# Performance work log

Hardware: AMD Instinct MI355X
Metric: run time of the kernel (lower is better)

The kernel has to match this reference:

```python
import jax, jax.numpy as jnp
import numpy as np


def _gcn_conv(x, src, dst, W, b, num_nodes, deg_inv_sqrt):
    # PyG GCNConv: h = x @ W, then normalized scatter-add over edges (incl. self loops), + bias
    h = x @ W  # [N, d_out]
    norm = deg_inv_sqrt[src] * deg_inv_sqrt[dst]  # [E']
    msg = h[src] * norm[:, None]  # gather + scale, [E', d_out]
    out = jax.ops.segment_sum(msg, dst, num_segments=num_nodes)  # scatter-add to targets
    return out + b


def reference(x, edge_index, W1, b1, W2, b2, num_nodes):
    src0, dst0 = edge_index[0], edge_index[1]
    loop = jnp.arange(num_nodes, dtype=edge_index.dtype)
    # add self loops (PyG default add_self_loops=True)
    src = jnp.concatenate([src0, loop])
    dst = jnp.concatenate([dst0, loop])
    # symmetric normalization D^{-1/2} (A+I) D^{-1/2}, degree from self-looped graph
    deg = jax.ops.segment_sum(jnp.ones_like(src, dtype=x.dtype), dst, num_segments=num_nodes)
    deg_inv_sqrt = jnp.where(deg > 0, jax.lax.rsqrt(jnp.maximum(deg, 1)), 0.0).astype(x.dtype)

    z = jax.nn.relu(_gcn_conv(x, src, dst, W1, b1, num_nodes, deg_inv_sqrt))
    z = jax.nn.relu(_gcn_conv(z, src, dst, W2, b2, num_nodes, deg_inv_sqrt))
    return z


def setup_inputs() -> dict:
    key = jax.random.key(0)
    k1, k2, k3, k4 = jax.random.split(key, 4)
    N, E, D, H = 50000, 1600000, 128, 128
    x = jax.random.normal(k1, (N, D), dtype=jnp.float32)
    edge_index = jax.random.randint(k2, (2, E), 0, N, dtype=jnp.int64)
    s = 1.0 / np.sqrt(D)
    W1 = jax.random.normal(k3, (D, H), dtype=jnp.float32) * s
    W2 = jax.random.normal(k4, (H, H), dtype=jnp.float32) * s
    return {
        "x": x,
        "edge_index": edge_index,
        "W1": W1,
        "b1": jnp.zeros((H,), jnp.float32),
        "W2": W2,
        "b2": jnp.zeros((H,), jnp.float32),
        "num_nodes": N,
    }
```

## Files before the change

### kernel.cpp

```cpp
#include <hip/hip_runtime.h>

#define FD 128
#define BSH 7
#define CH 4096
#define CHT 16
#define KMAX 512
#define SCAP 8192

typedef __attribute__((ext_vector_type(8))) short bf16x8;
typedef __attribute__((ext_vector_type(4))) float f32x4;

__device__ inline unsigned bfr(float f) {
    unsigned u = __float_as_uint(f);
    return (u + 0x7FFF + ((u >> 16) & 1)) >> 16;
}
__device__ inline float uplo(unsigned p) { return __uint_as_float(p << 16); }
__device__ inline float uphi(unsigned p) { return __uint_as_float(p & 0xFFFF0000u); }


__global__ __launch_bounds__(256) void partition_kernel(
        const int* __restrict__ src, const int* __restrict__ dst,
        int* __restrict__ lstartG, int* __restrict__ total,
        int* __restrict__ pairs, int E, int K) {
    __shared__ int lcnt[KMAX];
    __shared__ int lstart[KMAX];
    __shared__ int sm[256];
    __shared__ int staged[CH];
    int t = threadIdx.x;
    int base = blockIdx.x * CH;
    int n = min(CH, E - base);

    lcnt[t] = 0; lcnt[t + 256] = 0;
    __syncthreads();

    int pk[CHT]; int bn[CHT];
    #pragma unroll
    for (int j = 0; j < CHT; ++j) {
        int i = t + j * 256;
        bn[j] = -1;
        if (i < n) {
            int d = dst[base + i];
            int s = src[base + i];
            bn[j] = d >> BSH;
            pk[j] = ((d & ((1 << BSH) - 1)) << 17) | s;
            atomicAdd(&lcnt[bn[j]], 1);
        }
    }
    __syncthreads();

    int c0 = lcnt[2 * t], c1 = lcnt[2 * t + 1];
    int s2 = c0 + c1;
    sm[t] = s2;
    __syncthreads();
    for (int off = 1; off < 256; off <<= 1) {
        int add = (t >= off) ? sm[t - off] : 0;
        __syncthreads();
        sm[t] += add;
        __syncthreads();
    }
    int ex = sm[t] - s2;
    lstart[2 * t] = ex;     lstart[2 * t + 1] = ex + c0;
    lcnt[2 * t]   = ex;     lcnt[2 * t + 1]   = ex + c0;
    __syncthreads();

    #pragma unroll
    for (int j = 0; j < CHT; ++j) {
        if (bn[j] >= 0) {
            int pos = atomicAdd(&lcnt[bn[j]], 1);
            staged[pos] = pk[j];
        }
    }
    __syncthreads();

    for (int i = t; i < n; i += 256)
        pairs[base + i] = staged[i];

    size_t lrow = (size_t)blockIdx.x * (K + 1);
    for (int b = t; b < K; b += 256) {
        lstartG[lrow + b] = lstart[b];
        int c = lcnt[b] - lstart[b];
        if (c) atomicAdd(&total[b], c);
    }
    if (t == 0) lstartG[lrow + K] = n;
}

__global__ __launch_bounds__(512) void trtot_kernel(
        const int* __restrict__ A, int* __restrict__ B, int R, int C,
        const int* __restrict__ total, int* __restrict__ bbase,
        int* __restrict__ rp, int K, int E, int N, int nbx) {
    __shared__ int tile[32][33];
    int t = threadIdx.x;
    if ((int)blockIdx.x == gridDim.x - 1) {
        __shared__ int sm[512];
        int v = (t < K) ? total[t] : 0;
        sm[t] = v;
        __syncthreads();
        for (int off = 1; off < 512; off <<= 1) {
            int add = (t >= off) ? sm[t - off] : 0;
            __syncthreads();
            sm[t] += add;
            __syncthreads();
        }
        if (t < K) bbase[t] = sm[t] - v;
        if (t == 0) { bbase[K] = E; rp[N] = E; }
        return;
    }
    int c0 = (blockIdx.x % nbx) * 32, r0 = (blockIdx.x / nbx) * 32;
    int tx = t & 31, ty = t >> 5;
    for (int i = ty; i < 32; i += 16) {
        int r = r0 + i, c = c0 + tx;
        if (r < R && c < C) tile[i][tx] = A[(size_t)r * C + c];
    }
    __syncthreads();
    for (int i = ty; i < 32; i += 16) {
        int c = c0 + i, r = r0 + tx;
        if (c < C && r < R) B[(size_t)c * R + r] = tile[tx][i];
    }
}

__global__ __launch_bounds__(256) void build_kernel(
        const int* __restrict__ pairs, const int* __restrict__ lstartT,
        const int* __restrict__ bbase, int* __restrict__ rp,
        float* __restrict__ dis, int* __restrict__ col, int N, int PB, int K,
        const float* __restrict__ W1, unsigned short* __restrict__ W1T,
        const float* __restrict__ W2, unsigned short* __restrict__ W2T) {
    __shared__ int staged[SCAP];
    __shared__ int lcnt[512];
    __shared__ int pref[512];
    __shared__ int sm[256];
    int b = blockIdx.x;
    int t = threadIdx.x;

    if (b >= K) {
        int bb = b - K;
        #pragma unroll
        for (int rr = 0; rr < 2; ++rr) {
            int f = bb * 512 + rr * 256 + t;
            int w = f >> 14, rm = f & 16383, k = rm >> 7, nn2 = rm & 127;
            const float* W = w ? W2 : W1;
            unsigned short* WT = w ? W2T : W1T;
            WT[nn2 * FD + k] = (unsigned short)bfr(W[k * FD + nn2]);
        }
        return;
    }

    int wv = t >> 6;
    int nbase = b << BSH;
    int nn = min(1 << BSH, N - nbase);
    int beg = bbase[b];
    int cnt = bbase[b + 1] - beg;

    int fp[2], fl0[2], flen[2];
    int nf = 0, mysum = 0;
    for (int p = t; p < PB; p += 256) {
        int l0 = lstartT[(size_t)b * PB + p];
        int l1 = lstartT[(size_t)(b + 1) * PB + p];
        fp[nf] = p; fl0[nf] = l0; flen[nf] = l1 - l0;
        mysum += l1 - l0;
        ++nf;
    }
    sm[t] = mysum;
    __syncthreads();
    for (int off = 1; off < 256; off <<= 1) {
        int add = (t >= off) ? sm[t - off] : 0;
        __syncthreads();
        sm[t] += add;
        __syncthreads();
    }
    int o = sm[t] - mysum;

    lcnt[t] = 0; lcnt[t + 256] = 0;
    __syncthreads();

    if (cnt <= SCAP) {
        int oo = o;
        for (int f = 0; f < nf; ++f) {
            int gbase = fp[f] * CH + fl0[f];
            for (int i = 0; i < flen[f]; ++i) {
                int p = pairs[gbase + i];
                staged[oo + i] = p;
                atomicAdd(&lcnt[((p >> 17) << 2) | wv], 1);
            }
            oo += flen[f];
        }
    } else {
        for (int f = 0; f < nf; ++f) {
            int gbase = fp[f] * CH + fl0[f];
            for (int i = 0; i < flen[f]; ++i)
                atomicAdd(&lcnt[((pairs[gbase + i] >> 17) << 2) | wv], 1);
        }
    }
    __syncthreads();

    int c0 = lcnt[2 * t], c1 = lcnt[2 * t + 1];
    int s2 = c0 + c1;
    sm[t] = s2;
    __syncthreads();
    for (int off = 1; off < 256; off <<= 1) {
        int add = (t >= off) ? sm[t - off] : 0;
        __syncthreads();
        sm[t] += add;
        __syncthreads();
    }
    int ex = sm[t] - s2;
    pref[2 * t] = ex;  pref[2 * t + 1] = ex + c0;
    __syncthreads();

    if (t < 128 && t < nn) {
        int rs = pref[t << 2];
        int re = (t < 127) ? pref[(t + 1) << 2] : cnt;
        rp[nbase + t] = beg + rs;
        dis[nbase + t] = rsqrtf((float)(re - rs + 1));
    }
    lcnt[2 * t]     = beg + pref[2 * t];
    lcnt[2 * t + 1] = beg + pref[2 * t + 1];
    __syncthreads();

    if (cnt <= SCAP) {
        int oo = o;
        for (int f = 0; f < nf; ++f) {
            for (int i = 0; i < flen[f]; ++i) {
                int p = staged[oo + i];
                int pos = atomicAdd(&lcnt[((p >> 17) << 2) | wv], 1);
                col[pos] = p & 0x1FFFF;
            }
            oo += flen[f];
        }
    } else {
        for (int f = 0; f < nf; ++f) {
            int gbase = fp[f] * CH + fl0[f];
            for (int i = 0; i < flen[f]; ++i) {
                int p = pairs[gbase + i];
                int pos = atomicAdd(&lcnt[((p >> 17) << 2) | wv], 1);
                col[pos] = p & 0x1FFFF;
            }
        }
    }
}


#define APAD 8
#define ASTR (FD + APAD)

template <bool A32>
__device__ void gemm_body(const void* __restrict__ Ap,
                          const unsigned short* __restrict__ WT,
                          const float* __restrict__ dis,
                          unsigned short* __restrict__ C, int M) {
    __shared__ unsigned short Bs[128 * ASTR];
    int tid = threadIdx.x;
    int lane = tid & 63;
    int wave = tid >> 6;
    int quad = lane >> 4;
    int l16 = lane & 15;
    int rowBase = blockIdx.x * 128;

    #pragma unroll
    for (int p = 0; p < 8; ++p) {
        int r = p * 16 + (tid >> 4);
        int cq = (tid & 15) * 8;
        *(uint4*)&Bs[r * ASTR + cq] = *(const uint4*)&WT[(size_t)r * FD + cq];
    }
    __syncthreads();

    int m0 = wave * 32;
    int r0 = rowBase + m0 + l16;
    int r1 = r0 + 16;
    f32x4 acc[2][8] = {};
    #pragma unroll
    for (int kt = 0; kt < 4; ++kt) {
        int ko = kt * 32 + quad * 8;
        uint4 va = make_uint4(0u, 0u, 0u, 0u);
        uint4 vb = make_uint4(0u, 0u, 0u, 0u);
        if (A32) {
            const float* A = (const float*)Ap;
            if (r0 < M) {
                const float* a = A + (size_t)r0 * FD + ko;
                float4 f0 = *(const float4*)a;
                float4 f1 = *(const float4*)(a + 4);
                va.x = bfr(f0.x) | (bfr(f0.y) << 16);
                va.y = bfr(f0.z) | (bfr(f0.w) << 16);
                va.z = bfr(f1.x) | (bfr(f1.y) << 16);
                va.w = bfr(f1.z) | (bfr(f1.w) << 16);
            }
            if (r1 < M) {
                const float* a = A + (size_t)r1 * FD + ko;
                float4 f0 = *(const float4*)a;
                float4 f1 = *(const float4*)(a + 4);
                vb.x = bfr(f0.x) | (bfr(f0.y) << 16);
                vb.y = bfr(f0.z) | (bfr(f0.w) << 16);
                vb.z = bfr(f1.x) | (bfr(f1.y) << 16);
                vb.w = bfr(f1.z) | (bfr(f1.w) << 16);
            }
        } else {
            const unsigned short* A = (const unsigned short*)Ap;
            if (r0 < M) va = *(const uint4*)(A + (size_t)r0 * FD + ko);
            if (r1 < M) vb = *(const uint4*)(A + (size_t)r1 * FD + ko);
        }
        bf16x8 a0 = *(bf16x8*)&va;
        bf16x8 a1 = *(bf16x8*)&vb;
        #pragma unroll
        for (int n = 0; n < 8; ++n) {
            bf16x8 b = *(bf16x8*)&Bs[(n * 16 + l16) * ASTR + ko];
            acc[0][n] = __builtin_amdgcn_mfma_f32_16x16x32_bf16(a0, b, acc[0][n], 0, 0, 0);
            acc[1][n] = __builtin_amdgcn_mfma_f32_16x16x32_bf16(a1, b, acc[1][n], 0, 0, 0);
        }
    }

    #pragma unroll
    for (int ms = 0; ms < 2; ++ms) {
        #pragma unroll
        for (int r = 0; r < 4; ++r) {
            int grow = rowBase + m0 + ms * 16 + quad * 4 + r;
            if (grow < M) {
                float dv = dis[grow];
                #pragma unroll
                for (int n = 0; n < 8; ++n) {
                    C[(size_t)grow * FD + n * 16 + l16] =
                        (unsigned short)bfr(dv * acc[ms][n][r]);
                }
            }
        }
    }
}

__global__ __launch_bounds__(256) void gemm_mfma_f32(
        const float* __restrict__ A, const unsigned short* __restrict__ WT,
        const float* __restrict__ dis, unsigned short* __restrict__ C, int M) {
    gemm_body<true>(A, WT, dis, C, M);
}

__global__ __launch_bounds__(256) void gemm_mfma_bf16(
        const unsigned short* __restrict__ A, const unsigned short* __restrict__ WT,
        const float* __restrict__ dis, unsigned short* __restrict__ C, int M) {
    gemm_body<false>(A, WT, dis, C, M);
}


__global__ __launch_bounds__(256) void agg_kernel(
        const unsigned* __restrict__ h, const float* __restrict__ dis,
        const int* __restrict__ rp, const int* __restrict__ col,
        const float2* __restrict__ bias, void* __restrict__ out, int N, int obf) {
    int v = blockIdx.x * 4 + threadIdx.y;
    v = __builtin_amdgcn_readfirstlane(v);
    if (v >= N) return;
    int t = threadIdx.x;
    float dv = dis[v];
    size_t vb = (size_t)v * 64 + t;
    unsigned hp = h[vb];
    float2 acc;
    acc.x = uplo(hp); acc.y = uphi(hp);
    int e = rp[v];
    int end = rp[v + 1];

    for (; e + 16 <= end; e += 16) {
        int u[16];
        #pragma unroll
        for (int j = 0; j < 16; ++j) u[j] = col[e + j];
        unsigned p[16];
        #pragma unroll
        for (int j = 0; j < 16; ++j) p[j] = h[(size_t)u[j] * 64 + t];
        #pragma unroll
        for (int j = 0; j < 16; ++j) {
            acc.x += uplo(p[j]); acc.y += uphi(p[j]);
        }
    }
    for (; e + 4 <= end; e += 4) {
        int u0 = col[e], u1 = col[e + 1], u2 = col[e + 2], u3 = col[e + 3];
        unsigned p0 = h[(size_t)u0 * 64 + t];
        unsigned p1 = h[(size_t)u1 * 64 + t];
        unsigned p2 = h[(size_t)u2 * 64 + t];
        unsigned p3 = h[(size_t)u3 * 64 + t];
        acc.x += uplo(p0); acc.y += uphi(p0);
        acc.x += uplo(p1); acc.y += uphi(p1);
        acc.x += uplo(p2); acc.y += uphi(p2);
        acc.x += uplo(p3); acc.y += uphi(p3);
    }
    for (; e < end; ++e) {
        unsigned p = h[(size_t)col[e] * 64 + t];
        acc.x += uplo(p); acc.y += uphi(p);
    }

    float2 bb = bias[t];
    float2 r;
    r.x = fmaxf(fmaf(dv, acc.x, bb.x), 0.0f);
    r.y = fmaxf(fmaf(dv, acc.y, bb.y), 0.0f);
    if (obf) {
        ((unsigned*)out)[vb] = bfr(r.x) | (bfr(r.y) << 16);
    } else {
        ((float2*)out)[vb] = r;
    }
}


extern "C" void kernel_launch(void* const* d_in, const int* in_sizes, int n_in,
                              void* d_out, int out_size, void* d_ws, size_t ws_size,
                              hipStream_t stream) {
    const float* x  = (const float*)d_in[0];
    const int*   ei = (const int*)d_in[1];
    const float* W1 = (const float*)d_in[2];
    const float* b1 = (const float*)d_in[3];
    const float* W2 = (const float*)d_in[4];
    const float* b2 = (const float*)d_in[5];

    int N = in_sizes[0] / FD;
    int E = in_sizes[1] / 2;
    const int* src = ei;
    const int* dst = ei + E;
    int K = (N + (1 << BSH) - 1) >> BSH;
    int PB = (E + CH - 1) / CH;

    char* base = (char*)d_ws;
    size_t off = 0;
    auto align256 = [](size_t v) { return (v + 255) & ~(size_t)255; };
    int*            rp    = (int*)(base + off);            off += align256((size_t)(N + 1) * 4);
    float*          dis   = (float*)(base + off);          off += align256((size_t)N * 4);
    int*            total = (int*)(base + off);            off += align256(512 * 4);
    int*            bbase = (int*)(base + off);            off += align256(513 * 4);
    unsigned short* w1t   = (unsigned short*)(base + off); off += align256((size_t)FD * FD * 2);
    unsigned short* w2t   = (unsigned short*)(base + off); off += align256((size_t)FD * FD * 2);
    int*            col   = (int*)(base + off);            off += align256((size_t)E * 4);
    unsigned short* hbuf  = (unsigned short*)(base + off); off += align256((size_t)N * FD * 2);
    unsigned short* z1    = (unsigned short*)(base + off); off += align256((size_t)N * FD * 2);
    int*            pairs = (int*)(base + off);            off += align256((size_t)E * 4);
    int*            lstartG = (int*)hbuf;
    int*            lstartT = (int*)z1;
    (void)ws_size; (void)n_in; (void)out_size;

    (void)hipMemsetAsync(total, 0, 512 * 4, stream);
    partition_kernel<<<PB, 256, 0, stream>>>(src, dst, lstartG, total, pairs, E, K);
    int nbx = (K + 1 + 31) / 32;
    int nby = (PB + 31) / 32;
    trtot_kernel<<<nbx * nby + 1, 512, 0, stream>>>(lstartG, lstartT, PB, K + 1,
                                                    total, bbase, rp, K, E, N, nbx);
    build_kernel<<<K + 64, 256, 0, stream>>>(pairs, lstartT, bbase, rp, dis, col,
                                             N, PB, K, W1, w1t, W2, w2t);

    dim3 aggBlk(64, 4);
    int aggGrid = (N + 3) / 4;
    int gemmGrid = (N + 127) / 128;

    gemm_mfma_f32 <<<gemmGrid, 256, 0, stream>>>(x, w1t, dis, hbuf, N);
    agg_kernel<<<aggGrid, aggBlk, 0, stream>>>((const unsigned*)hbuf, dis, rp, col,
                                               (const float2*)b1, z1, N, 1);
    gemm_mfma_bf16<<<gemmGrid, 256, 0, stream>>>(z1, w2t, dis, hbuf, N);
    agg_kernel<<<aggGrid, aggBlk, 0, stream>>>((const unsigned*)hbuf, dis, rp, col,
                                               (const float2*)b2, d_out, N, 0);
}
```

Baseline: 245.4 us.

## Compute degrees with atomics and fuse layer-1 GEMM into CSR build kernel

Node degrees are now counted with global atomics in extra blocks of the partition kernel, and the inverse square roots plus the weight transposes move into extra blocks of the transpose kernel. Because the normalisation no longer depends on the CSR build, the first-layer GEMM runs as extra blocks of the build kernel, so it overlaps the column scatter and one launch is removed. In exchange it adds 1.6M random global atomics and a larger memset. The GEMM blocks also inherit the build kernel's bigger shared-memory allocation, which may lower their occupancy.

```diff
diff --git a/kernel.cpp b/kernel.cpp
--- a/kernel.cpp
+++ b/kernel.cpp
@@ -6,6 +6,7 @@
 #define CHT 16
 #define KMAX 512
 #define SCAP 8192
+#define DB 128
 
 typedef __attribute__((ext_vector_type(8))) short bf16x8;
 typedef __attribute__((ext_vector_type(4))) float f32x4;
@@ -21,12 +22,21 @@
 __global__ __launch_bounds__(256) void partition_kernel(
         const int* __restrict__ src, const int* __restrict__ dst,
         int* __restrict__ lstartG, int* __restrict__ total,
-        int* __restrict__ pairs, int E, int K) {
+        int* __restrict__ pairs, int E, int K, int PB,
+        int* __restrict__ deg) {
     __shared__ int lcnt[KMAX];
     __shared__ int lstart[KMAX];
     __shared__ int sm[256];
     __shared__ int staged[CH];
     int t = threadIdx.x;
+
+    if ((int)blockIdx.x >= PB) {
+        int i0 = ((int)blockIdx.x - PB) * 256 + t;
+        for (int i = i0; i < E; i += DB * 256)
+            atomicAdd(&deg[dst[i]], 1);
+        return;
+    }
+
     int base = blockIdx.x * CH;
     int n = min(CH, E - base);
 
@@ -87,10 +97,14 @@
 __global__ __launch_bounds__(512) void trtot_kernel(
         const int* __restrict__ A, int* __restrict__ B, int R, int C,
         const int* __restrict__ total, int* __restrict__ bbase,
-        int* __restrict__ rp, int K, int E, int N, int nbx) {
+        int* __restrict__ rp, int K, int E, int N, int nbx, int nbt, int ndis,
+        const int* __restrict__ deg, float* __restrict__ dis,
+        const float* __restrict__ W1, unsigned short* __restrict__ W1T,
+        const float* __restrict__ W2, unsigned short* __restrict__ W2T) {
     __shared__ int tile[32][33];
     int t = threadIdx.x;
-    if ((int)blockIdx.x == gridDim.x - 1) {
+    int b = blockIdx.x;
+    if (b == nbt) {
         __shared__ int sm[512];
         int v = (t < K) ? total[t] : 0;
         sm[t] = v;
@@ -105,7 +119,21 @@
         if (t == 0) { bbase[K] = E; rp[N] = E; }
         return;
     }
-    int c0 = (blockIdx.x % nbx) * 32, r0 = (blockIdx.x / nbx) * 32;
+    if (b > nbt) {
+        int i = b - nbt - 1;
+        if (i < ndis) {
+            int v = i * 512 + t;
+            if (v < N) dis[v] = rsqrtf((float)(deg[v] + 1));
+        } else {
+            int f = (i - ndis) * 512 + t;
+            int w = f >> 14, rm = f & 16383, k = rm >> 7, nn2 = rm & 127;
+            const float* W = w ? W2 : W1;
+            unsigned short* WT = w ? W2T : W1T;
+            WT[nn2 * FD + k] = (unsigned short)bfr(W[k * FD + nn2]);
+        }
+        return;
+    }
+    int c0 = (b % nbx) * 32, r0 = (b / nbx) * 32;
     int tx = t & 31, ty = t >> 5;
     for (int i = ty; i < 32; i += 16) {
         int r = r0 + i, c = c0 + tx;
@@ -118,142 +146,22 @@
     }
 }
 
-__global__ __launch_bounds__(256) void build_kernel(
-        const int* __restrict__ pairs, const int* __restrict__ lstartT,
-        const int* __restrict__ bbase, int* __restrict__ rp,
-        float* __restrict__ dis, int* __restrict__ col, int N, int PB, int K,
-        const float* __restrict__ W1, unsigned short* __restrict__ W1T,
-        const float* __restrict__ W2, unsigned short* __restrict__ W2T) {
-    __shared__ int staged[SCAP];
-    __shared__ int lcnt[512];
-    __shared__ int pref[512];
-    __shared__ int sm[256];
-    int b = blockIdx.x;
-    int t = threadIdx.x;
-
-    if (b >= K) {
-        int bb = b - K;
-        #pragma unroll
-        for (int rr = 0; rr < 2; ++rr) {
-            int f = bb * 512 + rr * 256 + t;
-            int w = f >> 14, rm = f & 16383, k = rm >> 7, nn2 = rm & 127;
-            const float* W = w ? W2 : W1;
-            unsigned short* WT = w ? W2T : W1T;
-            WT[nn2 * FD + k] = (unsigned short)bfr(W[k * FD + nn2]);
-        }
-        return;
-    }
-
-    int wv = t >> 6;
-    int nbase = b << BSH;
-    int nn = min(1 << BSH, N - nbase);
-    int beg = bbase[b];
-    int cnt = bbase[b + 1] - beg;
-
-    int fp[2], fl0[2], flen[2];
-    int nf = 0, mysum = 0;
-    for (int p = t; p < PB; p += 256) {
-        int l0 = lstartT[(size_t)b * PB + p];
-        int l1 = lstartT[(size_t)(b + 1) * PB + p];
-        fp[nf] = p; fl0[nf] = l0; flen[nf] = l1 - l0;
-        mysum += l1 - l0;
-        ++nf;
-    }
-    sm[t] = mysum;
-    __syncthreads();
-    for (int off = 1; off < 256; off <<= 1) {
-        int add = (t >= off) ? sm[t - off] : 0;
-        __syncthreads();
-        sm[t] += add;
-        __syncthreads();
-    }
-    int o = sm[t] - mysum;
-
-    lcnt[t] = 0; lcnt[t + 256] = 0;
-    __syncthreads();
-
-    if (cnt <= SCAP) {
-        int oo = o;
-        for (int f = 0; f < nf; ++f) {
-            int gbase = fp[f] * CH + fl0[f];
-            for (int i = 0; i < flen[f]; ++i) {
-                int p = pairs[gbase + i];
-                staged[oo + i] = p;
-                atomicAdd(&lcnt[((p >> 17) << 2) | wv], 1);
-            }
-            oo += flen[f];
-        }
-    } else {
-        for (int f = 0; f < nf; ++f) {
-            int gbase = fp[f] * CH + fl0[f];
-            for (int i = 0; i < flen[f]; ++i)
-                atomicAdd(&lcnt[((pairs[gbase + i] >> 17) << 2) | wv], 1);
-        }
-    }
-    __syncthreads();
-
-    int c0 = lcnt[2 * t], c1 = lcnt[2 * t + 1];
-    int s2 = c0 + c1;
-    sm[t] = s2;
-    __syncthreads();
-    for (int off = 1; off < 256; off <<= 1) {
-        int add = (t >= off) ? sm[t - off] : 0;
-        __syncthreads();
-        sm[t] += add;
-        __syncthreads();
-    }
-    int ex = sm[t] - s2;
-    pref[2 * t] = ex;  pref[2 * t + 1] = ex + c0;
-    __syncthreads();
-
-    if (t < 128 && t < nn) {
-        int rs = pref[t << 2];
-        int re = (t < 127) ? pref[(t + 1) << 2] : cnt;
-        rp[nbase + t] = beg + rs;
-        dis[nbase + t] = rsqrtf((float)(re - rs + 1));
-    }
-    lcnt[2 * t]     = beg + pref[2 * t];
-    lcnt[2 * t + 1] = beg + pref[2 * t + 1];
-    __syncthreads();
-
-    if (cnt <= SCAP) {
-        int oo = o;
-        for (int f = 0; f < nf; ++f) {
-            for (int i = 0; i < flen[f]; ++i) {
-                int p = staged[oo + i];
-                int pos = atomicAdd(&lcnt[((p >> 17) << 2) | wv], 1);
-                col[pos] = p & 0x1FFFF;
-            }
-            oo += flen[f];
-        }
-    } else {
-        for (int f = 0; f < nf; ++f) {
-            int gbase = fp[f] * CH + fl0[f];
-            for (int i = 0; i < flen[f]; ++i) {
-                int p = pairs[gbase + i];
-                int pos = atomicAdd(&lcnt[((p >> 17) << 2) | wv], 1);
-                col[pos] = p & 0x1FFFF;
-            }
-        }
-    }
-}
-
 
 #define APAD 8
 #define ASTR (FD + APAD)
 
 template <bool A32>
-__device__ void gemm_body(const void* __restrict__ Ap,
+__device__ void gemm_body(unsigned short* __restrict__ Bs,
+                          const void* __restrict__ Ap,
                           const unsigned short* __restrict__ WT,
                           const float* __restrict__ dis,
-                          unsigned short* __restrict__ C, int M) {
-    __shared__ unsigned short Bs[128 * ASTR];
+                          unsigned short* __restrict__ C, int M, int blk) {
     int tid = threadIdx.x;
     int lane = tid & 63;
     int wave = tid >> 6;
     int quad = lane >> 4;
     int l16 = lane & 15;
-    int rowBase = blockIdx.x * 128;
+    int rowBase = blk * 128;
 
     #pragma unroll
     for (int p = 0; p < 8; ++p) {
@@ -324,16 +232,123 @@
     }
 }
 
-__global__ __launch_bounds__(256) void gemm_mfma_f32(
-        const float* __restrict__ A, const unsigned short* __restrict__ WT,
-        const float* __restrict__ dis, unsigned short* __restrict__ C, int M) {
-    gemm_body<true>(A, WT, dis, C, M);
+__global__ __launch_bounds__(256) void build_kernel(
+        const int* __restrict__ pairs, const int* __restrict__ lstartT,
+        const int* __restrict__ bbase, int* __restrict__ rp,
+        int* __restrict__ col, int N, int PB, int K,
+        const float* __restrict__ x, const unsigned short* __restrict__ w1t,
+        const float* __restrict__ dis, unsigned short* __restrict__ hbuf) {
+    __shared__ __align__(16) int smem[SCAP + 512 + 512 + 256];
+    int b = blockIdx.x;
+    int t = threadIdx.x;
+
+    if (b >= K) {
+        gemm_body<true>((unsigned short*)smem, x, w1t, dis, hbuf, N, b - K);
+        return;
+    }
+
+    int* staged = smem;
+    int* lcnt   = smem + SCAP;
+    int* pref   = smem + SCAP + 512;
+    int* sm     = smem + SCAP + 1024;
+
+    int wv = t >> 6;
+    int nbase = b << BSH;
+    int nn = min(1 << BSH, N - nbase);
+    int beg = bbase[b];
+    int cnt = bbase[b + 1] - beg;
+
+    int fp[2], fl0[2], flen[2];
+    int nf = 0, mysum = 0;
+    for (int p = t; p < PB; p += 256) {
+        int l0 = lstartT[(size_t)b * PB + p];
+        int l1 = lstartT[(size_t)(b + 1) * PB + p];
+        fp[nf] = p; fl0[nf] = l0; flen[nf] = l1 - l0;
+        mysum += l1 - l0;
+        ++nf;
+    }
+    sm[t] = mysum;
+    __syncthreads();
+    for (int off = 1; off < 256; off <<= 1) {
+        int add = (t >= off) ? sm[t - off] : 0;
+        __syncthreads();
+        sm[t] += add;
+        __syncthreads();
+    }
+    int o = sm[t] - mysum;
+
+    lcnt[t] = 0; lcnt[t + 256] = 0;
+    __syncthreads();
+
+    if (cnt <= SCAP) {
+        int oo = o;
+        for (int f = 0; f < nf; ++f) {
+            int gbase = fp[f] * CH + fl0[f];
+            for (int i = 0; i < flen[f]; ++i) {
+                int p = pairs[gbase + i];
+                staged[oo + i] = p;
+                atomicAdd(&lcnt[((p >> 17) << 2) | wv], 1);
+            }
+            oo += flen[f];
+        }
+    } else {
+        for (int f = 0; f < nf; ++f) {
+            int gbase = fp[f] * CH + fl0[f];
+            for (int i = 0; i < flen[f]; ++i)
+                atomicAdd(&lcnt[((pairs[gbase + i] >> 17) << 2) | wv], 1);
+        }
+    }
+    __syncthreads();
+
+    int c0 = lcnt[2 * t], c1 = lcnt[2 * t + 1];
+    int s2 = c0 + c1;
+    sm[t] = s2;
+    __syncthreads();
+    for (int off = 1; off < 256; off <<= 1) {
+        int add = (t >= off) ? sm[t - off] : 0;
+        __syncthreads();
+        sm[t] += add;
+        __syncthreads();
+    }
+    int ex = sm[t] - s2;
+    pref[2 * t] = ex;  pref[2 * t + 1] = ex + c0;
+    __syncthreads();
+
+    if (t < 128 && t < nn) {
+        int rs = pref[t << 2];
+        rp[nbase + t] = beg + rs;
+    }
+    lcnt[2 * t]     = beg + pref[2 * t];
+    lcnt[2 * t + 1] = beg + pref[2 * t + 1];
+    __syncthreads();
+
+    if (cnt <= SCAP) {
+        int oo = o;
+        for (int f = 0; f < nf; ++f) {
+            for (int i = 0; i < flen[f]; ++i) {
+                int p = staged[oo + i];
+                int pos = atomicAdd(&lcnt[((p >> 17) << 2) | wv], 1);
+                col[pos] = p & 0x1FFFF;
+            }
+            oo += flen[f];
+        }
+    } else {
+        for (int f = 0; f < nf; ++f) {
+            int gbase = fp[f] * CH + fl0[f];
+            for (int i = 0; i < flen[f]; ++i) {
+                int p = pairs[gbase + i];
+                int pos = atomicAdd(&lcnt[((p >> 17) << 2) | wv], 1);
+                col[pos] = p & 0x1FFFF;
+            }
+        }
+    }
 }
 
 __global__ __launch_bounds__(256) void gemm_mfma_bf16(
         const unsigned short* __restrict__ A, const unsigned short* __restrict__ WT,
         const float* __restrict__ dis, unsigned short* __restrict__ C, int M) {
-    gemm_body<false>(A, WT, dis, C, M);
+    __shared__ __align__(16) unsigned short Bs[128 * ASTR];
+    gemm_body<false>(Bs, A, WT, dis, C, M, blockIdx.x);
 }
 
 
@@ -416,6 +431,7 @@
     int*            rp    = (int*)(base + off);            off += align256((size_t)(N + 1) * 4);
     float*          dis   = (float*)(base + off);          off += align256((size_t)N * 4);
     int*            total = (int*)(base + off);            off += align256(512 * 4);
+    int*            deg   = (int*)(base + off);            off += align256((size_t)N * 4);
     int*            bbase = (int*)(base + off);            off += align256(513 * 4);
     unsigned short* w1t   = (unsigned short*)(base + off); off += align256((size_t)FD * FD * 2);
     unsigned short* w2t   = (unsigned short*)(base + off); off += align256((size_t)FD * FD * 2);
@@ -427,20 +443,25 @@
     int*            lstartT = (int*)z1;
     (void)ws_size; (void)n_in; (void)out_size;
 
-    (void)hipMemsetAsync(total, 0, 512 * 4, stream);
-    partition_kernel<<<PB, 256, 0, stream>>>(src, dst, lstartG, total, pairs, E, K);
+    (void)hipMemsetAsync(total, 0, 2048 + (size_t)N * 4, stream);
+    partition_kernel<<<PB + DB, 256, 0, stream>>>(src, dst, lstartG, total,
+                                                  pairs, E, K, PB, deg);
     int nbx = (K + 1 + 31) / 32;
     int nby = (PB + 31) / 32;
-    trtot_kernel<<<nbx * nby + 1, 512, 0, stream>>>(lstartG, lstartT, PB, K + 1,
-                                                    total, bbase, rp, K, E, N, nbx);
-    build_kernel<<<K + 64, 256, 0, stream>>>(pairs, lstartT, bbase, rp, dis, col,
-                                             N, PB, K, W1, w1t, W2, w2t);
+    int nbt = nbx * nby;
+    int ndis = (N + 511) / 512;
+    trtot_kernel<<<nbt + 1 + ndis + 64, 512, 0, stream>>>(
+        lstartG, lstartT, PB, K + 1, total, bbase, rp, K, E, N, nbx, nbt, ndis,
+        deg, dis, W1, w1t, W2, w2t);
+
+    int gemmGrid = (N + 127) / 128;
+    build_kernel<<<K + gemmGrid, 256, 0, stream>>>(pairs, lstartT, bbase, rp,
+                                                   col, N, PB, K,
+                                                   x, w1t, dis, hbuf);
 
     dim3 aggBlk(64, 4);
     int aggGrid = (N + 3) / 4;
-    int gemmGrid = (N + 127) / 128;
-
-    gemm_mfma_f32 <<<gemmGrid, 256, 0, stream>>>(x, w1t, dis, hbuf, N);
+
     agg_kernel<<<aggGrid, aggBlk, 0, stream>>>((const unsigned*)hbuf, dis, rp, col,
                                                (const float2*)b1, z1, N, 1);
     gemm_mfma_bf16<<<gemmGrid, 256, 0, stream>>>(z1, w2t, dis, hbuf, N);
```

After: 300.0 us. 1.22x slower.

## Fuse layer-1 GEMM into partition kernel and move degree scaling into aggregation

Applied to the files above, without the earlier changes.

The first-layer GEMM no longer needs the degree normalization, because the source-side scale is applied per edge inside the first aggregation (gathering dis[u] alongside h). That lets the x@W1 GEMM run as extra blocks in the same launch as edge partitioning, overlapping compute with the graph build. The weight transpose moves to a small separate kernel, and lstartG gets its own workspace region instead of aliasing hbuf. In exchange, the first aggregation does an extra random dis load and an FMA per edge, and the bf16 rounding of h now happens before scaling.

```diff
diff --git a/kernel.cpp b/kernel.cpp
--- a/kernel.cpp
+++ b/kernel.cpp
@@ -18,242 +18,21 @@
 __device__ inline float uphi(unsigned p) { return __uint_as_float(p & 0xFFFF0000u); }
 
 
-__global__ __launch_bounds__(256) void partition_kernel(
-        const int* __restrict__ src, const int* __restrict__ dst,
-        int* __restrict__ lstartG, int* __restrict__ total,
-        int* __restrict__ pairs, int E, int K) {
-    __shared__ int lcnt[KMAX];
-    __shared__ int lstart[KMAX];
-    __shared__ int sm[256];
-    __shared__ int staged[CH];
-    int t = threadIdx.x;
-    int base = blockIdx.x * CH;
-    int n = min(CH, E - base);
-
-    lcnt[t] = 0; lcnt[t + 256] = 0;
-    __syncthreads();
-
-    int pk[CHT]; int bn[CHT];
-    #pragma unroll
-    for (int j = 0; j < CHT; ++j) {
-        int i = t + j * 256;
-        bn[j] = -1;
-        if (i < n) {
-            int d = dst[base + i];
-            int s = src[base + i];
-            bn[j] = d >> BSH;
-            pk[j] = ((d & ((1 << BSH) - 1)) << 17) | s;
-            atomicAdd(&lcnt[bn[j]], 1);
-        }
-    }
-    __syncthreads();
-
-    int c0 = lcnt[2 * t], c1 = lcnt[2 * t + 1];
-    int s2 = c0 + c1;
-    sm[t] = s2;
-    __syncthreads();
-    for (int off = 1; off < 256; off <<= 1) {
-        int add = (t >= off) ? sm[t - off] : 0;
-        __syncthreads();
-        sm[t] += add;
-        __syncthreads();
-    }
-    int ex = sm[t] - s2;
-    lstart[2 * t] = ex;     lstart[2 * t + 1] = ex + c0;
-    lcnt[2 * t]   = ex;     lcnt[2 * t + 1]   = ex + c0;
-    __syncthreads();
-
-    #pragma unroll
-    for (int j = 0; j < CHT; ++j) {
-        if (bn[j] >= 0) {
-            int pos = atomicAdd(&lcnt[bn[j]], 1);
-            staged[pos] = pk[j];
-        }
-    }
-    __syncthreads();
-
-    for (int i = t; i < n; i += 256)
-        pairs[base + i] = staged[i];
-
-    size_t lrow = (size_t)blockIdx.x * (K + 1);
-    for (int b = t; b < K; b += 256) {
-        lstartG[lrow + b] = lstart[b];
-        int c = lcnt[b] - lstart[b];
-        if (c) atomicAdd(&total[b], c);
-    }
-    if (t == 0) lstartG[lrow + K] = n;
-}
-
-__global__ __launch_bounds__(512) void trtot_kernel(
-        const int* __restrict__ A, int* __restrict__ B, int R, int C,
-        const int* __restrict__ total, int* __restrict__ bbase,
-        int* __restrict__ rp, int K, int E, int N, int nbx) {
-    __shared__ int tile[32][33];
-    int t = threadIdx.x;
-    if ((int)blockIdx.x == gridDim.x - 1) {
-        __shared__ int sm[512];
-        int v = (t < K) ? total[t] : 0;
-        sm[t] = v;
-        __syncthreads();
-        for (int off = 1; off < 512; off <<= 1) {
-            int add = (t >= off) ? sm[t - off] : 0;
-            __syncthreads();
-            sm[t] += add;
-            __syncthreads();
-        }
-        if (t < K) bbase[t] = sm[t] - v;
-        if (t == 0) { bbase[K] = E; rp[N] = E; }
-        return;
-    }
-    int c0 = (blockIdx.x % nbx) * 32, r0 = (blockIdx.x / nbx) * 32;
-    int tx = t & 31, ty = t >> 5;
-    for (int i = ty; i < 32; i += 16) {
-        int r = r0 + i, c = c0 + tx;
-        if (r < R && c < C) tile[i][tx] = A[(size_t)r * C + c];
-    }
-    __syncthreads();
-    for (int i = ty; i < 32; i += 16) {
-        int c = c0 + i, r = r0 + tx;
-        if (c < C && r < R) B[(size_t)c * R + r] = tile[tx][i];
-    }
-}
-
-__global__ __launch_bounds__(256) void build_kernel(
-        const int* __restrict__ pairs, const int* __restrict__ lstartT,
-        const int* __restrict__ bbase, int* __restrict__ rp,
-        float* __restrict__ dis, int* __restrict__ col, int N, int PB, int K,
-        const float* __restrict__ W1, unsigned short* __restrict__ W1T,
-        const float* __restrict__ W2, unsigned short* __restrict__ W2T) {
-    __shared__ int staged[SCAP];
-    __shared__ int lcnt[512];
-    __shared__ int pref[512];
-    __shared__ int sm[256];
-    int b = blockIdx.x;
-    int t = threadIdx.x;
-
-    if (b >= K) {
-        int bb = b - K;
-        #pragma unroll
-        for (int rr = 0; rr < 2; ++rr) {
-            int f = bb * 512 + rr * 256 + t;
-            int w = f >> 14, rm = f & 16383, k = rm >> 7, nn2 = rm & 127;
-            const float* W = w ? W2 : W1;
-            unsigned short* WT = w ? W2T : W1T;
-            WT[nn2 * FD + k] = (unsigned short)bfr(W[k * FD + nn2]);
-        }
-        return;
-    }
-
-    int wv = t >> 6;
-    int nbase = b << BSH;
-    int nn = min(1 << BSH, N - nbase);
-    int beg = bbase[b];
-    int cnt = bbase[b + 1] - beg;
-
-    int fp[2], fl0[2], flen[2];
-    int nf = 0, mysum = 0;
-    for (int p = t; p < PB; p += 256) {
-        int l0 = lstartT[(size_t)b * PB + p];
-        int l1 = lstartT[(size_t)(b + 1) * PB + p];
-        fp[nf] = p; fl0[nf] = l0; flen[nf] = l1 - l0;
-        mysum += l1 - l0;
-        ++nf;
-    }
-    sm[t] = mysum;
-    __syncthreads();
-    for (int off = 1; off < 256; off <<= 1) {
-        int add = (t >= off) ? sm[t - off] : 0;
-        __syncthreads();
-        sm[t] += add;
-        __syncthreads();
-    }
-    int o = sm[t] - mysum;
-
-    lcnt[t] = 0; lcnt[t + 256] = 0;
-    __syncthreads();
-
-    if (cnt <= SCAP) {
-        int oo = o;
-        for (int f = 0; f < nf; ++f) {
-            int gbase = fp[f] * CH + fl0[f];
-            for (int i = 0; i < flen[f]; ++i) {
-                int p = pairs[gbase + i];
-                staged[oo + i] = p;
-                atomicAdd(&lcnt[((p >> 17) << 2) | wv], 1);
-            }
-            oo += flen[f];
-        }
-    } else {
-        for (int f = 0; f < nf; ++f) {
-            int gbase = fp[f] * CH + fl0[f];
-            for (int i = 0; i < flen[f]; ++i)
-                atomicAdd(&lcnt[((pairs[gbase + i] >> 17) << 2) | wv], 1);
-        }
-    }
-    __syncthreads();
-
-    int c0 = lcnt[2 * t], c1 = lcnt[2 * t + 1];
-    int s2 = c0 + c1;
-    sm[t] = s2;
-    __syncthreads();
-    for (int off = 1; off < 256; off <<= 1) {
-        int add = (t >= off) ? sm[t - off] : 0;
-        __syncthreads();
-        sm[t] += add;
-        __syncthreads();
-    }
-    int ex = sm[t] - s2;
-    pref[2 * t] = ex;  pref[2 * t + 1] = ex + c0;
-    __syncthreads();
-
-    if (t < 128 && t < nn) {
-        int rs = pref[t << 2];
-        int re = (t < 127) ? pref[(t + 1) << 2] : cnt;
-        rp[nbase + t] = beg + rs;
-        dis[nbase + t] = rsqrtf((float)(re - rs + 1));
-    }
-    lcnt[2 * t]     = beg + pref[2 * t];
-    lcnt[2 * t + 1] = beg + pref[2 * t + 1];
-    __syncthreads();
-
-    if (cnt <= SCAP) {
-        int oo = o;
-        for (int f = 0; f < nf; ++f) {
-            for (int i = 0; i < flen[f]; ++i) {
-                int p = staged[oo + i];
-                int pos = atomicAdd(&lcnt[((p >> 17) << 2) | wv], 1);
-                col[pos] = p & 0x1FFFF;
-            }
-            oo += flen[f];
-        }
-    } else {
-        for (int f = 0; f < nf; ++f) {
-            int gbase = fp[f] * CH + fl0[f];
-            for (int i = 0; i < flen[f]; ++i) {
-                int p = pairs[gbase + i];
-                int pos = atomicAdd(&lcnt[((p >> 17) << 2) | wv], 1);
-                col[pos] = p & 0x1FFFF;
-            }
-        }
-    }
-}
-
-
 #define APAD 8
 #define ASTR (FD + APAD)
 
-template <bool A32>
-__device__ void gemm_body(const void* __restrict__ Ap,
+template <bool A32, bool SCALE>
+__device__ void gemm_body(unsigned short* __restrict__ Bs,
+                          const void* __restrict__ Ap,
                           const unsigned short* __restrict__ WT,
                           const float* __restrict__ dis,
-                          unsigned short* __restrict__ C, int M) {
-    __shared__ unsigned short Bs[128 * ASTR];
+                          unsigned short* __restrict__ C, int M, int blk) {
     int tid = threadIdx.x;
     int lane = tid & 63;
     int wave = tid >> 6;
     int quad = lane >> 4;
     int l16 = lane & 15;
-    int rowBase = blockIdx.x * 128;
+    int rowBase = blk * 128;
 
     #pragma unroll
     for (int p = 0; p < 8; ++p) {
@@ -313,34 +92,253 @@
         for (int r = 0; r < 4; ++r) {
             int grow = rowBase + m0 + ms * 16 + quad * 4 + r;
             if (grow < M) {
-                float dv = dis[grow];
+                float dv = SCALE ? dis[grow] : 1.0f;
                 #pragma unroll
                 for (int n = 0; n < 8; ++n) {
-                    C[(size_t)grow * FD + n * 16 + l16] =
-                        (unsigned short)bfr(dv * acc[ms][n][r]);
+                    float val = SCALE ? (dv * acc[ms][n][r]) : acc[ms][n][r];
+                    C[(size_t)grow * FD + n * 16 + l16] = (unsigned short)bfr(val);
                 }
             }
         }
     }
 }
 
-__global__ __launch_bounds__(256) void gemm_mfma_f32(
-        const float* __restrict__ A, const unsigned short* __restrict__ WT,
-        const float* __restrict__ dis, unsigned short* __restrict__ C, int M) {
-    gemm_body<true>(A, WT, dis, C, M);
+__global__ void wt_kernel(const float* __restrict__ W1, unsigned short* __restrict__ W1T,
+                          const float* __restrict__ W2, unsigned short* __restrict__ W2T) {
+    int k = blockIdx.x & (FD - 1);
+    int n = threadIdx.x;
+    if (blockIdx.x < FD) W1T[n * FD + k] = (unsigned short)bfr(W1[k * FD + n]);
+    else                 W2T[n * FD + k] = (unsigned short)bfr(W2[k * FD + n]);
+}
+
+__global__ __launch_bounds__(256) void part_gemm_kernel(
+        const int* __restrict__ src, const int* __restrict__ dst,
+        int* __restrict__ lstartG, int* __restrict__ total,
+        int* __restrict__ pairs, int E, int K, int PB,
+        const float* __restrict__ x, const unsigned short* __restrict__ w1t,
+        unsigned short* __restrict__ hbuf, int N) {
+    __shared__ __align__(16) int smem[8704];
+    int t = threadIdx.x;
+
+    if ((int)blockIdx.x >= PB) {
+        gemm_body<true, false>((unsigned short*)smem, x, w1t, nullptr, hbuf,
+                               N, (int)blockIdx.x - PB);
+        return;
+    }
+
+    int* lcnt   = smem;
+    int* lstart = smem + 512;
+    int* sm     = smem + 1024;
+    int* staged = smem + 1280;
+
+    int base = blockIdx.x * CH;
+    int n = min(CH, E - base);
+
+    lcnt[t] = 0; lcnt[t + 256] = 0;
+    __syncthreads();
+
+    int pk[CHT]; int bn[CHT];
+    #pragma unroll
+    for (int j = 0; j < CHT; ++j) {
+        int i = t + j * 256;
+        bn[j] = -1;
+        if (i < n) {
+            int d = dst[base + i];
+            int s = src[base + i];
+            bn[j] = d >> BSH;
+            pk[j] = ((d & ((1 << BSH) - 1)) << 17) | s;
+            atomicAdd(&lcnt[bn[j]], 1);
+        }
+    }
+    __syncthreads();
+
+    int c0 = lcnt[2 * t], c1 = lcnt[2 * t + 1];
+    int s2 = c0 + c1;
+    sm[t] = s2;
+    __syncthreads();
+    for (int off = 1; off < 256; off <<= 1) {
+        int add = (t >= off) ? sm[t - off] : 0;
+        __syncthreads();
+        sm[t] += add;
+        __syncthreads();
+    }
+    int ex = sm[t] - s2;
+    lstart[2 * t] = ex;     lstart[2 * t + 1] = ex + c0;
+    lcnt[2 * t]   = ex;     lcnt[2 * t + 1]   = ex + c0;
+    __syncthreads();
+
+    #pragma unroll
+    for (int j = 0; j < CHT; ++j) {
+        if (bn[j] >= 0) {
+            int pos = atomicAdd(&lcnt[bn[j]], 1);
+            staged[pos] = pk[j];
+        }
+    }
+    __syncthreads();
+
+    for (int i = t; i < n; i += 256)
+        pairs[base + i] = staged[i];
+
+    size_t lrow = (size_t)blockIdx.x * (K + 1);
+    for (int b = t; b < K; b += 256) {
+        lstartG[lrow + b] = lstart[b];
+        int c = lcnt[b] - lstart[b];
+        if (c) atomicAdd(&total[b], c);
+    }
+    if (t == 0) lstartG[lrow + K] = n;
+}
+
+__global__ __launch_bounds__(512) void trtot_kernel(
+        const int* __restrict__ A, int* __restrict__ B, int R, int C,
+        const int* __restrict__ total, int* __restrict__ bbase,
+        int* __restrict__ rp, int K, int E, int N, int nbx) {
+    __shared__ int tile[32][33];
+    int t = threadIdx.x;
+    if ((int)blockIdx.x == gridDim.x - 1) {
+        __shared__ int sm[512];
+        int v = (t < K) ? total[t] : 0;
+        sm[t] = v;
+        __syncthreads();
+        for (int off = 1; off < 512; off <<= 1) {
+            int add = (t >= off) ? sm[t - off] : 0;
+            __syncthreads();
+            sm[t] += add;
+            __syncthreads();
+        }
+        if (t < K) bbase[t] = sm[t] - v;
+        if (t == 0) { bbase[K] = E; rp[N] = E; }
+        return;
+    }
+    int c0 = (blockIdx.x % nbx) * 32, r0 = (blockIdx.x / nbx) * 32;
+    int tx = t & 31, ty = t >> 5;
+    for (int i = ty; i < 32; i += 16) {
+        int r = r0 + i, c = c0 + tx;
+        if (r < R && c < C) tile[i][tx] = A[(size_t)r * C + c];
+    }
+    __syncthreads();
+    for (int i = ty; i < 32; i += 16) {
+        int c = c0 + i, r = r0 + tx;
+        if (c < C && r < R) B[(size_t)c * R + r] = tile[tx][i];
+    }
+}
+
+__global__ __launch_bounds__(256) void build_kernel(
+        const int* __restrict__ pairs, const int* __restrict__ lstartT,
+        const int* __restrict__ bbase, int* __restrict__ rp,
+        float* __restrict__ dis, int* __restrict__ col, int N, int PB, int K) {
+    __shared__ int staged[SCAP];
+    __shared__ int lcnt[512];
+    __shared__ int pref[512];
+    __shared__ int sm[256];
+    int b = blockIdx.x;
+    int t = threadIdx.x;
+    int wv = t >> 6;
+    int nbase = b << BSH;
+    int nn = min(1 << BSH, N - nbase);
+    int beg = bbase[b];
+    int cnt = bbase[b + 1] - beg;
+
+    int fp[2], fl0[2], flen[2];
+    int nf = 0, mysum = 0;
+    for (int p = t; p < PB; p += 256) {
+        int l0 = lstartT[(size_t)b * PB + p];
+        int l1 = lstartT[(size_t)(b + 1) * PB + p];
+        fp[nf] = p; fl0[nf] = l0; flen[nf] = l1 - l0;
+        mysum += l1 - l0;
+        ++nf;
+    }
+    sm[t] = mysum;
+    __syncthreads();
+    for (int off = 1; off < 256; off <<= 1) {
+        int add = (t >= off) ? sm[t - off] : 0;
+        __syncthreads();
+        sm[t] += add;
+        __syncthreads();
+    }
+    int o = sm[t] - mysum;
+
+    lcnt[t] = 0; lcnt[t + 256] = 0;
+    __syncthreads();
+
+    if (cnt <= SCAP) {
+        int oo = o;
+        for (int f = 0; f < nf; ++f) {
+            int gbase = fp[f] * CH + fl0[f];
+            for (int i = 0; i < flen[f]; ++i) {
+                int p = pairs[gbase + i];
+                staged[oo + i] = p;
+                atomicAdd(&lcnt[((p >> 17) << 2) | wv], 1);
+            }
+            oo += flen[f];
+        }
+    } else {
+        for (int f = 0; f < nf; ++f) {
+            int gbase = fp[f] * CH + fl0[f];
+            for (int i = 0; i < flen[f]; ++i)
+                atomicAdd(&lcnt[((pairs[gbase + i] >> 17) << 2) | wv], 1);
+        }
+    }
+    __syncthreads();
+
+    int c0 = lcnt[2 * t], c1 = lcnt[2 * t + 1];
+    int s2 = c0 + c1;
+    sm[t] = s2;
+    __syncthreads();
+    for (int off = 1; off < 256; off <<= 1) {
+        int add = (t >= off) ? sm[t - off] : 0;
+        __syncthreads();
+        sm[t] += add;
+        __syncthreads();
+    }
+    int ex = sm[t] - s2;
+    pref[2 * t] = ex;  pref[2 * t + 1] = ex + c0;
+    __syncthreads();
+
+    if (t < 128 && t < nn) {
+        int rs = pref[t << 2];
+        int re = (t < 127) ? pref[(t + 1) << 2] : cnt;
+        rp[nbase + t] = beg + rs;
+        dis[nbase + t] = rsqrtf((float)(re - rs + 1));
+    }
+    lcnt[2 * t]     = beg + pref[2 * t];
+    lcnt[2 * t + 1] = beg + pref[2 * t + 1];
+    __syncthreads();
+
+    if (cnt <= SCAP) {
+        int oo = o;
+        for (int f = 0; f < nf; ++f) {
+            for (int i = 0; i < flen[f]; ++i) {
+                int p = staged[oo + i];
+                int pos = atomicAdd(&lcnt[((p >> 17) << 2) | wv], 1);
+                col[pos] = p & 0x1FFFF;
+            }
+            oo += flen[f];
+        }
+    } else {
+        for (int f = 0; f < nf; ++f) {
+            int gbase = fp[f] * CH + fl0[f];
+            for (int i = 0; i < flen[f]; ++i) {
+                int p = pairs[gbase + i];
+                int pos = atomicAdd(&lcnt[((p >> 17) << 2) | wv], 1);
+                col[pos] = p & 0x1FFFF;
+            }
+        }
+    }
 }
 
 __global__ __launch_bounds__(256) void gemm_mfma_bf16(
         const unsigned short* __restrict__ A, const unsigned short* __restrict__ WT,
         const float* __restrict__ dis, unsigned short* __restrict__ C, int M) {
-    gemm_body<false>(A, WT, dis, C, M);
-}
-
-
-__global__ __launch_bounds__(256) void agg_kernel(
-        const unsigned* __restrict__ h, const float* __restrict__ dis,
-        const int* __restrict__ rp, const int* __restrict__ col,
-        const float2* __restrict__ bias, void* __restrict__ out, int N, int obf) {
+    __shared__ __align__(16) unsigned short Bs[128 * ASTR];
+    gemm_body<false, true>(Bs, A, WT, dis, C, M, blockIdx.x);
+}
+
+
+template <bool ESCALE>
+__device__ void agg_body(const unsigned* __restrict__ h, const float* __restrict__ dis,
+                         const int* __restrict__ rp, const int* __restrict__ col,
+                         const float2* __restrict__ bias, void* __restrict__ out,
+                         int N, int obf) {
     int v = blockIdx.x * 4 + threadIdx.y;
     v = __builtin_amdgcn_readfirstlane(v);
     if (v >= N) return;
@@ -349,7 +347,8 @@
     size_t vb = (size_t)v * 64 + t;
     unsigned hp = h[vb];
     float2 acc;
-    acc.x = uplo(hp); acc.y = uphi(hp);
+    if (ESCALE) { acc.x = dv * uplo(hp); acc.y = dv * uphi(hp); }
+    else        { acc.x = uplo(hp);      acc.y = uphi(hp); }
     int e = rp[v];
     int end = rp[v + 1];
 
@@ -357,12 +356,22 @@
         int u[16];
         #pragma unroll
         for (int j = 0; j < 16; ++j) u[j] = col[e + j];
+        float du[16];
+        if (ESCALE) {
+            #pragma unroll
+            for (int j = 0; j < 16; ++j) du[j] = dis[u[j]];
+        }
         unsigned p[16];
         #pragma unroll
         for (int j = 0; j < 16; ++j) p[j] = h[(size_t)u[j] * 64 + t];
         #pragma unroll
         for (int j = 0; j < 16; ++j) {
-            acc.x += uplo(p[j]); acc.y += uphi(p[j]);
+            if (ESCALE) {
+                acc.x = fmaf(du[j], uplo(p[j]), acc.x);
+                acc.y = fmaf(du[j], uphi(p[j]), acc.y);
+            } else {
+                acc.x += uplo(p[j]); acc.y += uphi(p[j]);
+            }
         }
     }
     for (; e + 4 <= end; e += 4) {
@@ -371,14 +380,28 @@
         unsigned p1 = h[(size_t)u1 * 64 + t];
         unsigned p2 = h[(size_t)u2 * 64 + t];
         unsigned p3 = h[(size_t)u3 * 64 + t];
-        acc.x += uplo(p0); acc.y += uphi(p0);
-        acc.x += uplo(p1); acc.y += uphi(p1);
-        acc.x += uplo(p2); acc.y += uphi(p2);
-        acc.x += uplo(p3); acc.y += uphi(p3);
+        if (ESCALE) {
+            float d0 = dis[u0], d1 = dis[u1], d2 = dis[u2], d3 = dis[u3];
+            acc.x = fmaf(d0, uplo(p0), acc.x); acc.y = fmaf(d0, uphi(p0), acc.y);
+            acc.x = fmaf(d1, uplo(p1), acc.x); acc.y = fmaf(d1, uphi(p1), acc.y);
+            acc.x = fmaf(d2, uplo(p2), acc.x); acc.y = fmaf(d2, uphi(p2), acc.y);
+            acc.x = fmaf(d3, uplo(p3), acc.x); acc.y = fmaf(d3, uphi(p3), acc.y);
+        } else {
+            acc.x += uplo(p0); acc.y += uphi(p0);
+            acc.x += uplo(p1); acc.y += uphi(p1);
+            acc.x += uplo(p2); acc.y += uphi(p2);
+            acc.x += uplo(p3); acc.y += uphi(p3);
+        }
     }
     for (; e < end; ++e) {
-        unsigned p = h[(size_t)col[e] * 64 + t];
-        acc.x += uplo(p); acc.y += uphi(p);
+        int u0 = col[e];
+        unsigned p = h[(size_t)u0 * 64 + t];
+        if (ESCALE) {
+            float d0 = dis[u0];
+            acc.x = fmaf(d0, uplo(p), acc.x); acc.y = fmaf(d0, uphi(p), acc.y);
+        } else {
+            acc.x += uplo(p); acc.y += uphi(p);
+        }
     }
 
     float2 bb = bias[t];
@@ -390,6 +413,20 @@
     } else {
         ((float2*)out)[vb] = r;
     }
+}
+
+__global__ __launch_bounds__(256) void agg_kernel_e(
+        const unsigned* __restrict__ h, const float* __restrict__ dis,
+        const int* __restrict__ rp, const int* __restrict__ col,
+        const float2* __restrict__ bias, void* __restrict__ out, int N, int obf) {
+    agg_body<true>(h, dis, rp, col, bias, out, N, obf);
+}
+
+__global__ __launch_bounds__(256) void agg_kernel(
+        const unsigned* __restrict__ h, const float* __restrict__ dis,
+        const int* __restrict__ rp, const int* __restrict__ col,
+        const float2* __restrict__ bias, void* __restrict__ out, int N, int obf) {
+    agg_body<false>(h, dis, rp, col, bias, out, N, obf);
 }
 
 
@@ -423,26 +460,29 @@
     unsigned short* hbuf  = (unsigned short*)(base + off); off += align256((size_t)N * FD * 2);
     unsigned short* z1    = (unsigned short*)(base + off); off += align256((size_t)N * FD * 2);
     int*            pairs = (int*)(base + off);            off += align256((size_t)E * 4);
-    int*            lstartG = (int*)hbuf;
+    int*            lstartG = (int*)(base + off);          off += align256((size_t)PB * (K + 1) * 4);
     int*            lstartT = (int*)z1;
     (void)ws_size; (void)n_in; (void)out_size;
 
     (void)hipMemsetAsync(total, 0, 512 * 4, stream);
-    partition_kernel<<<PB, 256, 0, stream>>>(src, dst, lstartG, total, pairs, E, K);
+    wt_kernel<<<2 * FD, FD, 0, stream>>>(W1, w1t, W2, w2t);
+
+    int gemmGrid = (N + 127) / 128;
+    part_gemm_kernel<<<PB + gemmGrid, 256, 0, stream>>>(
+        src, dst, lstartG, total, pairs, E, K, PB, x, w1t, hbuf, N);
+
     int nbx = (K + 1 + 31) / 32;
     int nby = (PB + 31) / 32;
     trtot_kernel<<<nbx * nby + 1, 512, 0, stream>>>(lstartG, lstartT, PB, K + 1,
                                                     total, bbase, rp, K, E, N, nbx);
-    build_kernel<<<K + 64, 256, 0, stream>>>(pairs, lstartT, bbase, rp, dis, col,
-                                             N, PB, K, W1, w1t, W2, w2t);
+    build_kernel<<<K, 256, 0, stream>>>(pairs, lstartT, bbase, rp, dis, col,
+                                        N, PB, K);
 
     dim3 aggBlk(64, 4);
     int aggGrid = (N + 3) / 4;
-    int gemmGrid = (N + 127) / 128;
-
-    gemm_mfma_f32 <<<gemmGrid, 256, 0, stream>>>(x, w1t, dis, hbuf, N);
-    agg_kernel<<<aggGrid, aggBlk, 0, stream>>>((const unsigned*)hbuf, dis, rp, col,
-                                               (const float2*)b1, z1, N, 1);
+
+    agg_kernel_e<<<aggGrid, aggBlk, 0, stream>>>((const unsigned*)hbuf, dis, rp, col,
+                                                 (const float2*)b1, z1, N, 1);
     gemm_mfma_bf16<<<gemmGrid, 256, 0, stream>>>(z1, w2t, dis, hbuf, N);
     agg_kernel<<<aggGrid, aggBlk, 0, stream>>>((const unsigned*)hbuf, dis, rp, col,
                                                (const float2*)b2, d_out, N, 0);
```

Result: no change. 242.6 us (-1.1%).
